# Performance work log

Hardware: AMD Instinct MI355X
Metric: run time of the kernel (lower is better)

Reference implementation:

```python
import jax, jax.numpy as jnp
import numpy as np

B, H, S, DK, DV = 2, 16, 2048, 64, 64

def setup_inputs() -> dict:
    key = jax.random.key(0)
    kq, kk, kv, km = jax.random.split(key, 4)
    q = jax.random.normal(kq, (B, H, S, DK), dtype=jnp.float32)
    k = jax.random.normal(kk, (B, H, S, DK), dtype=jnp.float32)
    v = jax.random.normal(kv, (B, H, S, DV), dtype=jnp.float32)
    mask = jax.random.randint(km, (B, H, S, S), 0, 2).astype(jnp.bool_)
    return {"q": q, "k": k, "v": v, "mask": mask}

def reference(q, k, v, mask):
    d_k = q.shape[-1]
    # scores: [B, H, Sq, Sk]
    scores = jnp.einsum('bhqd,bhkd->bhqk', q, k) / np.sqrt(d_k).astype(jnp.float32)
    scores = jnp.where(mask, jnp.float32(-1e9), scores)
    attn = jax.nn.softmax(scores, axis=-1)
    return jnp.einsum('bhqk,bhkd->bhqd', attn, v)
```

## Files before the change

kernel.cpp:

```cpp
#include <hip/hip_runtime.h>


#define LOG2E 1.4426950408889634f
#define QSCALE (0.125f * LOG2E)

typedef __attribute__((ext_vector_type(8))) short short8;
typedef __attribute__((ext_vector_type(4))) short short4v;
typedef __attribute__((ext_vector_type(4))) float f32x4;
typedef unsigned __attribute__((ext_vector_type(4))) uintv4;

constexpr int S = 2048, D = 64;

__device__ __forceinline__ short bf16rne(float x) {
  union { float f; unsigned u; } cv; cv.f = x;
  unsigned u = cv.u;
  u += 0x7fffu + ((u >> 16) & 1u);
  return (short)(u >> 16);
}

__device__ __forceinline__ void glds16(const void* g, void* l) {
  __builtin_amdgcn_global_load_lds(
      (const __attribute__((address_space(1))) void*)g,
      (__attribute__((address_space(3))) void*)l, 16, 0, 0);
}

__global__ void prep(const float* __restrict__ kp, const float* __restrict__ vp,
                     short* __restrict__ kb, short* __restrict__ vt,
                     const unsigned* __restrict__ m, int* __restrict__ flag) {
  const int b = blockIdx.x;
  const int tid = threadIdx.x;
  if (b == 0 && tid < 64) {
    unsigned v = m[tid];
    unsigned long long big = __ballot(v > 1u && v != 0x3F800000u);
    unsigned long long isf = __ballot(v == 0x3F800000u);
    if (tid == 0) *flag = (big != 0ull && isf == 0ull) ? 1 : 0;
  }
  if (b < 2048) {
    size_t i = ((size_t)b * 256 + tid) * 8;
    float4 a = *(const float4*)(kp + i);
    float4 c = *(const float4*)(kp + i + 4);
    short8 s;
    s[0] = bf16rne(a.x); s[1] = bf16rne(a.y); s[2] = bf16rne(a.z); s[3] = bf16rne(a.w);
    s[4] = bf16rne(c.x); s[5] = bf16rne(c.y); s[6] = bf16rne(c.z); s[7] = bf16rne(c.w);
    *(short8*)&kb[i] = s;
  } else {
    __shared__ float tile[64][65];
    const int bb = b - 2048;
    const int bh = bb >> 5, k0 = (bb & 31) * 64;
    const float* src = vp + ((size_t)(bh * S + k0)) * D;
#pragma unroll
    for (int i = 0; i < 4; ++i) {
      int row = i * 16 + (tid >> 4);
      int col = (tid & 15) * 4;
      float4 x = *(const float4*)(src + row * D + col);
      tile[row][col] = x.x; tile[row][col + 1] = x.y;
      tile[row][col + 2] = x.z; tile[row][col + 3] = x.w;
    }
    __syncthreads();
#pragma unroll
    for (int i = 0; i < 4; ++i) {
      int dim = i * 16 + (tid >> 4);
      int kb4 = (tid & 15) * 4;
      short4v s;
#pragma unroll
      for (int j = 0; j < 4; ++j) s[j] = bf16rne(tile[kb4 + j][dim]);
      *(short4v*)&vt[((size_t)(bh * D + dim)) * S + k0 + kb4] = s;
    }
  }
}

__launch_bounds__(256, 4)
__global__ void attn_fwd(const float* __restrict__ qp, const short* __restrict__ kb,
                         const short* __restrict__ vt, const void* __restrict__ mp,
                         float* __restrict__ op, const int* __restrict__ fmtp) {
  const int fmt  = *fmtp;
  const int tid  = threadIdx.x;
  const int lane = tid & 63;
  const int w    = tid >> 6;
  const int c    = lane & 15;
  const int quad = lane >> 4;

  const int bh = blockIdx.x >> 5;
  const int q0 = (blockIdx.x & 31) * 64;

  __shared__ short ks[64 * 64];
  __shared__ short vs[64 * 64];
  __shared__ short pst[4][16 * 72];

  const float* qg = qp + ((size_t)(bh * S + q0 + w * 16 + c)) * D;
  short8 qB[2];
#pragma unroll
  for (int kk = 0; kk < 2; ++kk) {
    const float* p = qg + kk * 32 + quad * 8;
    float4 x = *(const float4*)(p);
    float4 y = *(const float4*)(p + 4);
    short8 f;
    f[0] = bf16rne(x.x * QSCALE); f[1] = bf16rne(x.y * QSCALE);
    f[2] = bf16rne(x.z * QSCALE); f[3] = bf16rne(x.w * QSCALE);
    f[4] = bf16rne(y.x * QSCALE); f[5] = bf16rne(y.y * QSCALE);
    f[6] = bf16rne(y.z * QSCALE); f[7] = bf16rne(y.w * QSCALE);
    qB[kk] = f;
  }

  f32x4 O[4];
#pragma unroll
  for (int t = 0; t < 4; ++t) O[t] = (f32x4){0.f, 0.f, 0.f, 0.f};
  float L = 0.f;

  const int rsub = lane >> 3;
  const int csw  = (lane & 7) ^ rsub;
  const short* kbase = kb + ((size_t)(bh * S)) * D;
  const short* vbase = vt + ((size_t)(bh * D)) * S;

  const int sw0 = ((quad    ) ^ (c & 7)) * 8;
  const int sw1 = ((quad | 4) ^ (c & 7)) * 8;

  const size_t mrow = ((size_t)(bh * S + q0 + w * 16 + c)) * S;

  uintv4  mr4[4];
  unsigned mr1[4];

  if (fmt == 1) {
    const unsigned char* mq = (const unsigned char*)mp + mrow + 4 * quad;
#pragma unroll
    for (int t = 0; t < 4; ++t)
      mr1[t] = __builtin_nontemporal_load((const unsigned*)(mq + 16 * t));
  } else {
    const unsigned* mq = (const unsigned*)mp + mrow + 4 * quad;
#pragma unroll
    for (int t = 0; t < 4; ++t)
      mr4[t] = __builtin_nontemporal_load((const uintv4*)(mq + 16 * t));
  }

  for (int it = 0; it < 32; ++it) {
    const int k0 = it * 64;
    __syncthreads();

#pragma unroll
    for (int h2 = 0; h2 < 2; ++h2) {
      const int row = (h2 * 4 + w) * 8 + rsub;
      glds16(kbase + (size_t)(k0 + row) * 64 + csw * 8,
             (char*)ks + (h2 * 4 + w) * 1024);
      glds16(vbase + (size_t)row * S + k0 + csw * 8,
             (char*)vs + (h2 * 4 + w) * 1024);
    }
    __syncthreads();

    unsigned mb[4];
    if (fmt == 1) {
#pragma unroll
      for (int t = 0; t < 4; ++t) mb[t] = mr1[t];
    } else {
#pragma unroll
      for (int t = 0; t < 4; ++t) {
        uintv4 v = mr4[t];
        mb[t] = (v[0] ? 1u : 0u) | (v[1] ? 0x100u : 0u) |
                (v[2] ? 0x10000u : 0u) | (v[3] ? 0x1000000u : 0u);
      }
    }

    if (it + 1 < 32) {
      const int k1 = (it + 1) * 64;
      if (fmt == 1) {
        const unsigned char* mq = (const unsigned char*)mp + mrow + k1 + 4 * quad;
#pragma unroll
        for (int t = 0; t < 4; ++t)
          mr1[t] = __builtin_nontemporal_load((const unsigned*)(mq + 16 * t));
      } else {
        const unsigned* mq = (const unsigned*)mp + mrow + k1 + 4 * quad;
#pragma unroll
        for (int t = 0; t < 4; ++t)
          mr4[t] = __builtin_nontemporal_load((const uintv4*)(mq + 16 * t));
      }
    }

    float part = 0.f;
#pragma unroll
    for (int t = 0; t < 4; ++t) {
      short8 ka0 = *(const short8*)&ks[(16 * t + c) * 64 + sw0];
      short8 ka1 = *(const short8*)&ks[(16 * t + c) * 64 + sw1];
      f32x4 z = (f32x4){0.f, 0.f, 0.f, 0.f};
      z = __builtin_amdgcn_mfma_f32_16x16x32_bf16(ka0, qB[0], z, 0, 0, 0);
      z = __builtin_amdgcn_mfma_f32_16x16x32_bf16(ka1, qB[1], z, 0, 0, 0);
      short4v s4;
#pragma unroll
      for (int r = 0; r < 4; ++r) {
        float e = ((mb[t] >> (8 * r)) & 0xffu) ? 0.f : exp2f(z[r]);
        part += e;
        s4[r] = bf16rne(e);
      }
      *(short4v*)&pst[w][c * 72 + 16 * t + 4 * quad] = s4;
    }

    part += __shfl_xor(part, 16);
    part += __shfl_xor(part, 32);
    L += part;

    short8 pa0 = *(const short8*)&pst[w][c * 72 + quad * 8];
    short8 pa1 = *(const short8*)&pst[w][c * 72 + 32 + quad * 8];
#pragma unroll
    for (int t = 0; t < 4; ++t) {
      short8 vb0 = *(const short8*)&vs[(16 * t + c) * 64 + sw0];
      short8 vb1 = *(const short8*)&vs[(16 * t + c) * 64 + sw1];
      O[t] = __builtin_amdgcn_mfma_f32_16x16x32_bf16(pa0, vb0, O[t], 0, 0, 0);
      O[t] = __builtin_amdgcn_mfma_f32_16x16x32_bf16(pa1, vb1, O[t], 0, 0, 0);
    }
  }

#pragma unroll
  for (int r = 0; r < 4; ++r) {
    float Lr = __shfl(L, (lane & 48) | (quad * 4 + r));
    float inv = 1.f / Lr;
    const size_t ob = ((size_t)(bh * S + q0 + w * 16 + quad * 4 + r)) * D;
#pragma unroll
    for (int t = 0; t < 4; ++t) op[ob + 16 * t + c] = O[t][r] * inv;
  }
}

extern "C" void kernel_launch(void* const* d_in, const int* in_sizes, int n_in,
                              void* d_out, int out_size, void* d_ws, size_t ws_size,
                              hipStream_t stream) {
  const float* q = (const float*)d_in[0];
  const float* k = (const float*)d_in[1];
  const float* v = (const float*)d_in[2];
  const void*  m = d_in[3];

  short* kbuf = (short*)d_ws;
  short* vtb  = (short*)((char*)d_ws + (8u << 20));
  int* flag   = (int*)((char*)d_ws + (16u << 20));

  prep<<<3072, 256, 0, stream>>>(k, v, kbuf, vtb, (const unsigned*)m, flag);
  attn_fwd<<<1024, 256, 0, stream>>>(q, kbuf, vtb, m, (float*)d_out, flag);
}
```

Measured before the change: 748.7 us.

## Keep P in registers by permuting V^T key order, drop LDS round-trip

Permutes the key order inside each 64-key block of the transposed V buffer so the MFMA output layout of the probability tile matches the operand layout needed by the PV MFMA. P no longer has to be staged through shared memory and re-read. It is packed directly into registers with a packed bf16 convert, and a faster mask-to-byte path is added for 0/1 integer masks. This removes LDS stores and loads plus their latency per iteration, at the cost of a tighter coupling between the prep layout and the kernel's register layout.

```diff
diff --git a/kernel.cpp b/kernel.cpp
--- a/kernel.cpp
+++ b/kernel.cpp
@@ -16,6 +16,15 @@
   unsigned u = cv.u;
   u += 0x7fffu + ((u >> 16) & 1u);
   return (short)(u >> 16);
+}
+
+__device__ __forceinline__ unsigned pkbf16(float a, float b) {
+#if __has_builtin(__builtin_amdgcn_cvt_pk_bf16_f32)
+  auto t = __builtin_amdgcn_cvt_pk_bf16_f32(a, b);
+  return __builtin_bit_cast(unsigned, t);
+#else
+  return ((unsigned)(unsigned short)bf16rne(b) << 16) | (unsigned short)bf16rne(a);
+#endif
 }
 
 __device__ __forceinline__ void glds16(const void* g, void* l) {
@@ -33,7 +42,8 @@
     unsigned v = m[tid];
     unsigned long long big = __ballot(v > 1u && v != 0x3F800000u);
     unsigned long long isf = __ballot(v == 0x3F800000u);
-    if (tid == 0) *flag = (big != 0ull && isf == 0ull) ? 1 : 0;
+    int f = (big != 0ull) ? 1 : ((isf != 0ull) ? 2 : 0);
+    if (tid == 0) *flag = f;
   }
   if (b < 2048) {
     size_t i = ((size_t)b * 256 + tid) * 8;
@@ -57,14 +67,16 @@
       tile[row][col + 2] = x.z; tile[row][col + 3] = x.w;
     }
     __syncthreads();
+    const int kblk = tid & 15;
+    const int t4 = kblk >> 2, q4 = kblk & 3;
+    const int p  = 8 * (t4 & 1) + 2 * q4 + (t4 >> 1);
 #pragma unroll
     for (int i = 0; i < 4; ++i) {
       int dim = i * 16 + (tid >> 4);
-      int kb4 = (tid & 15) * 4;
       short4v s;
 #pragma unroll
-      for (int j = 0; j < 4; ++j) s[j] = bf16rne(tile[kb4 + j][dim]);
-      *(short4v*)&vt[((size_t)(bh * D + dim)) * S + k0 + kb4] = s;
+      for (int j = 0; j < 4; ++j) s[j] = bf16rne(tile[kblk * 4 + j][dim]);
+      *(short4v*)&vt[((size_t)(bh * D + dim)) * S + k0 + 4 * p] = s;
     }
   }
 }
@@ -85,7 +97,6 @@
 
   __shared__ short ks[64 * 64];
   __shared__ short vs[64 * 64];
-  __shared__ short pst[4][16 * 72];
 
   const float* qg = qp + ((size_t)(bh * S + q0 + w * 16 + c)) * D;
   short8 qB[2];
@@ -150,6 +161,12 @@
     if (fmt == 1) {
 #pragma unroll
       for (int t = 0; t < 4; ++t) mb[t] = mr1[t];
+    } else if (fmt == 0) {
+#pragma unroll
+      for (int t = 0; t < 4; ++t) {
+        uintv4 v = mr4[t];
+        mb[t] = v[0] | (v[1] << 8) | (v[2] << 16) | (v[3] << 24);
+      }
     } else {
 #pragma unroll
       for (int t = 0; t < 4; ++t) {
@@ -175,6 +192,7 @@
     }
 
     float part = 0.f;
+    unsigned dA[4], dB[4];
 #pragma unroll
     for (int t = 0; t < 4; ++t) {
       short8 ka0 = *(const short8*)&ks[(16 * t + c) * 64 + sw0];
@@ -182,28 +200,31 @@
       f32x4 z = (f32x4){0.f, 0.f, 0.f, 0.f};
       z = __builtin_amdgcn_mfma_f32_16x16x32_bf16(ka0, qB[0], z, 0, 0, 0);
       z = __builtin_amdgcn_mfma_f32_16x16x32_bf16(ka1, qB[1], z, 0, 0, 0);
-      short4v s4;
+      float e[4];
 #pragma unroll
       for (int r = 0; r < 4; ++r) {
-        float e = ((mb[t] >> (8 * r)) & 0xffu) ? 0.f : exp2f(z[r]);
-        part += e;
-        s4[r] = bf16rne(e);
-      }
-      *(short4v*)&pst[w][c * 72 + 16 * t + 4 * quad] = s4;
+        e[r] = ((mb[t] >> (8 * r)) & 0xffu) ? 0.f : exp2f(z[r]);
+        part += e[r];
+      }
+      dA[t] = pkbf16(e[0], e[1]);
+      dB[t] = pkbf16(e[2], e[3]);
     }
 
     part += __shfl_xor(part, 16);
     part += __shfl_xor(part, 32);
     L += part;
 
-    short8 pa0 = *(const short8*)&pst[w][c * 72 + quad * 8];
-    short8 pa1 = *(const short8*)&pst[w][c * 72 + 32 + quad * 8];
+    uintv4 u0 = (uintv4){dA[0], dB[0], dA[2], dB[2]};
+    uintv4 u1 = (uintv4){dA[1], dB[1], dA[3], dB[3]};
+    short8 pB0 = __builtin_bit_cast(short8, u0);
+    short8 pB1 = __builtin_bit_cast(short8, u1);
+
 #pragma unroll
     for (int t = 0; t < 4; ++t) {
       short8 vb0 = *(const short8*)&vs[(16 * t + c) * 64 + sw0];
       short8 vb1 = *(const short8*)&vs[(16 * t + c) * 64 + sw1];
-      O[t] = __builtin_amdgcn_mfma_f32_16x16x32_bf16(pa0, vb0, O[t], 0, 0, 0);
-      O[t] = __builtin_amdgcn_mfma_f32_16x16x32_bf16(pa1, vb1, O[t], 0, 0, 0);
+      O[t] = __builtin_amdgcn_mfma_f32_16x16x32_bf16(pB0, vb0, O[t], 0, 0, 0);
+      O[t] = __builtin_amdgcn_mfma_f32_16x16x32_bf16(pB1, vb1, O[t], 0, 0, 0);
     }
   }
 
```

Result: no change. 750.2 us (+0.2%).
